# Optimization experiments

Hardware: AMD Instinct MI355X
Metric: run time of the kernel (lower is better)

Reference implementation:

```python
import jax, jax.numpy as jnp
import numpy as np

B, N = 128, 64
HID, MLP, DS, DV = 128, 128, 32, 32
DH = MLP - DS - DV  # 64
FILL = -10.0


def _embed_mask(x, W, b, fill):
    # Linear+ReLU on non-NaN rows; fill NaN rows with `fill` (matches embed_with_masking).
    nan = jnp.isnan(x).any(-1)
    e = jax.nn.relu(jnp.where(jnp.isnan(x), 0.0, x) @ W + b)
    return jnp.where(nan[..., None], jnp.asarray(fill, x.dtype), e)


def setup_inputs() -> dict:
    key = jax.random.key(0)
    ks = jax.random.split(key, 12)
    s = 0.05
    return {
        "hidden_states": jax.random.normal(ks[0], (B, N, HID), jnp.float32),
        "obs1": jax.random.normal(ks[1], (B, N, 2), jnp.float32),
        "obs2": jax.random.normal(ks[2], (B, N, 2), jnp.float32),
        "w_sp": jax.random.normal(ks[3], (2, DS), jnp.float32) * s,
        "b_sp": jnp.zeros((DS,), jnp.float32),
        "w_vel": jax.random.normal(ks[4], (2, DV), jnp.float32) * s,
        "b_vel": jnp.zeros((DV,), jnp.float32),
        "w_hid": jax.random.normal(ks[5], (HID, DH), jnp.float32) * s,
        "b_hid": jnp.zeros((DH,), jnp.float32),
        "wq": jax.random.normal(ks[6], (MLP, MLP), jnp.float32) * s,
        "wk": jax.random.normal(ks[7], (MLP, MLP), jnp.float32) * s,
        "wv": jax.random.normal(ks[8], (MLP, MLP), jnp.float32) * s,
        "in_proj_w": jax.random.normal(ks[9], (MLP, 3 * MLP), jnp.float32) * s,
        "in_proj_b": jnp.zeros((3 * MLP,), jnp.float32),
        "mha_out_w": jax.random.normal(ks[10], (MLP, MLP), jnp.float32) * s,
        "mha_out_b": jnp.zeros((MLP,), jnp.float32),
        "out_w": jax.random.normal(ks[11], (MLP, MLP), jnp.float32) * s,
        "out_b": jnp.zeros((MLP,), jnp.float32),
    }


def reference(hidden_states, obs1, obs2, w_sp, b_sp, w_vel, b_vel, w_hid, b_hid,
              wq, wk, wv, in_proj_w, in_proj_b, mha_out_w, mha_out_b, out_w, out_b):
    b, n = obs2.shape[0], obs2.shape[1]
    # relative positions: rel[b,i,j] = obs2[b,j] - obs2[b,i]
    rel = obs2[:, None, :, :] - obs2[:, :, None, :]              # [B,N,N,2]
    sp = _embed_mask(rel, w_sp, b_sp, FILL)                      # [B,N,N,DS]
    hid = _embed_mask(hidden_states, w_hid, b_hid, 0.0)          # [B,N,DH]
    hid_unf = jnp.broadcast_to(hid[:, None, :, :], (b, n, n, DH))
    vel = obs2 - obs1
    relvel = vel[:, None, :, :] - vel[:, :, None, :]             # [B,N,N,2]
    dv = _embed_mask(relvel * 4, w_vel, b_vel, FILL)             # [B,N,N,DV]
    emb = jnp.concatenate([sp, hid_unf, dv], axis=-1)            # [B,N,N,MLP]

    # MHA (1 head) in-proj weights split (stored as [in,out])
    w_iq, w_ik, w_iv = in_proj_w[:, :MLP], in_proj_w[:, MLP:2 * MLP], in_proj_w[:, 2 * MLP:]
    b_iq, b_ik, b_iv = in_proj_b[:MLP], in_proj_b[MLP:2 * MLP], in_proj_b[2 * MLP:]

    # Only the diagonal query position is kept by the final eye-mask gather,
    # and softmax rows are independent, so compute q only at j == i.
    idx = jnp.arange(n)
    emb_diag = emb[:, idx, idx]                                  # [B,N,MLP]
    q = (emb_diag @ wq) @ w_iq + b_iq                            # [B,N,MLP]
    k = (emb @ wk) @ w_ik + b_ik                                 # [B,N,N,MLP]
    v = (emb @ wv) @ w_iv + b_iv                                 # [B,N,N,MLP]

    scores = jnp.einsum('bid,bijd->bij', q, k) / jnp.sqrt(jnp.asarray(MLP, q.dtype))
    attn = jax.nn.softmax(scores, axis=-1)                       # [B,N,N]
    ctx = jnp.einsum('bij,bijd->bid', attn, v)                   # [B,N,MLP]
    mha_out = ctx @ mha_out_w + mha_out_b
    out = mha_out @ out_w + out_b                                # [B,N,out_dim]
    return out.reshape(b * n, -1)
```

## Files before the change

### kernel.cpp

```cpp
#include <hip/hip_runtime.h>

typedef float v2f __attribute__((ext_vector_type(2)));
#define PKFMA(a,b,c) __builtin_elementwise_fma((a),(b),(c))
#define PKMAX(a,b)   __builtin_elementwise_max((a),(b))
static __device__ __forceinline__ v2f vsplat(float s) { return (v2f){s, s}; }
static __device__ __forceinline__ v2f vmk(float a, float b) { return (v2f){a, b}; }
static __device__ __forceinline__ v2f shfl_xor_v2(v2f x, int m) {
    double d = __builtin_bit_cast(double, x);
    d = __shfl_xor(d, m, 64);
    return __builtin_bit_cast(v2f, d);
}

#define WS_WQC   0
#define WS_WKC   16384
#define WS_WVC   32768
#define WS_MOW   49152
#define WS_GQ    65536
#define WS_G0Q   73728
#define WS_FALL  73856
#define WS_FB    90240
#define WS_HID   90368
#define WS_NEED_HID_BYTES ((size_t)(90368 + 128*64*64) * 4)

__global__ __launch_bounds__(256) void precompute1(
    const float* __restrict__ wq, const float* __restrict__ wk,
    const float* __restrict__ wv, const float* __restrict__ in_proj_w,
    const float* __restrict__ mha_out_w, const float* __restrict__ out_w,
    const float* __restrict__ hs, const float* __restrict__ w_hid,
    const float* __restrict__ b_hid, float* __restrict__ ws)
{
    __shared__ __align__(16) float sbuf[4224];
    const int tid = threadIdx.x;

    if (blockIdx.x < 256) {
        const int mat  = blockIdx.x >> 6;
        const int rp   = blockIdx.x & 63;
        const int rsel = tid >> 7;
        const int col  = tid & 127;
        const int r    = 2 * rp + rsel;
        const float* A; const float* Bm; int ldb; float* C;
        if (mat == 0)      { A = wq;        Bm = in_proj_w;       ldb = 384; C = ws + WS_WQC; }
        else if (mat == 1) { A = wk;        Bm = in_proj_w + 128; ldb = 384; C = ws + WS_WKC; }
        else if (mat == 2) { A = wv;        Bm = in_proj_w + 256; ldb = 384; C = ws + WS_WVC; }
        else               { A = mha_out_w; Bm = out_w;           ldb = 128; C = ws + WS_MOW; }
        sbuf[tid] = A[r * 128 + col];
        __syncthreads();
        float acc = 0.f;
        #pragma unroll 8
        for (int d = 0; d < 128; ++d) acc = fmaf(sbuf[rsel * 128 + d], Bm[d * ldb + col], acc);
        C[r * 128 + col] = acc;
    } else {
        const int b2 = blockIdx.x - 256;
        const int b = b2 >> 1, half = b2 & 1;
        const float4* src = (const float4*)(hs + b * 8192 + half * 4096);
        for (int k = tid; k < 1024; k += 256) {
            const int row = k >> 5, c = k & 31;
            *(float4*)&sbuf[row * 132 + 4 * c] = src[k];
        }
        __syncthreads();
        const int ty = tid >> 4, tx = tid & 15;
        float a0c[4] = {0,0,0,0}, a1c[4] = {0,0,0,0};
        for (int d0 = 0; d0 < 128; d0 += 4) {
            const float4 a0 = *(const float4*)&sbuf[(2*ty+0)*132 + d0];
            const float4 a1 = *(const float4*)&sbuf[(2*ty+1)*132 + d0];
            const float* a0p = (const float*)&a0;
            const float* a1p = (const float*)&a1;
            #pragma unroll
            for (int dd = 0; dd < 4; ++dd) {
                const float4 w4 = *(const float4*)&w_hid[(d0+dd)*64 + 4*tx];
                a0c[0] = fmaf(a0p[dd], w4.x, a0c[0]); a0c[1] = fmaf(a0p[dd], w4.y, a0c[1]);
                a0c[2] = fmaf(a0p[dd], w4.z, a0c[2]); a0c[3] = fmaf(a0p[dd], w4.w, a0c[3]);
                a1c[0] = fmaf(a1p[dd], w4.x, a1c[0]); a1c[1] = fmaf(a1p[dd], w4.y, a1c[1]);
                a1c[2] = fmaf(a1p[dd], w4.z, a1c[2]); a1c[3] = fmaf(a1p[dd], w4.w, a1c[3]);
            }
        }
        const float4 bh = *(const float4*)&b_hid[4*tx];
        float* dst = ws + WS_HID + b * 4096 + (32*half + 2*ty) * 64 + 4*tx;
        *(float4*)dst        = make_float4(fmaxf(a0c[0]+bh.x,0.f), fmaxf(a0c[1]+bh.y,0.f),
                                           fmaxf(a0c[2]+bh.z,0.f), fmaxf(a0c[3]+bh.w,0.f));
        *(float4*)(dst + 64) = make_float4(fmaxf(a1c[0]+bh.x,0.f), fmaxf(a1c[1]+bh.y,0.f),
                                           fmaxf(a1c[2]+bh.z,0.f), fmaxf(a1c[3]+bh.w,0.f));
    }
}

__global__ __launch_bounds__(128) void precompute2(
    const float* __restrict__ b_sp, const float* __restrict__ b_vel,
    const float* __restrict__ in_proj_b, const float* __restrict__ mha_out_b,
    const float* __restrict__ out_w, const float* __restrict__ out_b,
    float* __restrict__ ws)
{
    const float* Wqc = ws + WS_WQC;
    const float* Wkc = ws + WS_WKC;
    const float* Wvc = ws + WS_WVC;
    const float* Mow = ws + WS_MOW;
    const int bid = blockIdx.x, tid = threadIdx.x;
    __shared__ __align__(16) float sa[128];

    if (bid < 64) {
        const int k = bid;
        sa[tid] = Wqc[(32 + k) * 128 + tid];
        __syncthreads();
        const int j = tid;
        const int pj = (j < 64) ? 32 + j : ((j < 96) ? j - 64 : j);
        const float* brow = Wkc + pj * 128;
        float acc = 0.f;
        #pragma unroll 8
        for (int d = 0; d < 128; d += 4) {
            const float4 a4 = *(const float4*)&sa[d];
            const float4 b4 = *(const float4*)&brow[d];
            acc = fmaf(a4.x, b4.x, fmaf(a4.y, b4.y, fmaf(a4.z, b4.z, fmaf(a4.w, b4.w, acc))));
        }
        ws[WS_GQ + k * 128 + j] = acc;
    } else if (bid < 192) {
        const int k2 = bid - 64;
        const int srcRow = (k2 < 32) ? k2 : ((k2 < 64) ? 96 + (k2 - 32) : 32 + (k2 - 64));
        sa[tid] = Wvc[srcRow * 128 + tid];
        __syncthreads();
        float acc = 0.f;
        #pragma unroll 8
        for (int m = 0; m < 128; ++m) acc = fmaf(sa[m], Mow[m * 128 + tid], acc);
        ws[WS_FALL + k2 * 128 + tid] = acc;
    } else if (bid == 192) {
        float acc = out_b[tid];
        #pragma unroll 8
        for (int m = 0; m < 128; ++m) {
            acc = fmaf(in_proj_b[256 + m], Mow[m * 128 + tid], acc);
            acc = fmaf(mha_out_b[m], out_w[m * 128 + tid], acc);
        }
        ws[WS_FB + tid] = acc;
    } else {
        float qc = in_proj_b[tid];
        #pragma unroll 4
        for (int s = 0; s < 32; ++s) {
            qc = fmaf(fmaxf(b_sp[s], 0.f),  Wqc[s * 128 + tid], qc);
            qc = fmaf(fmaxf(b_vel[s], 0.f), Wqc[(96 + s) * 128 + tid], qc);
        }
        sa[tid] = qc;
        __syncthreads();
        const int j = tid;
        const int pj = (j < 64) ? 32 + j : ((j < 96) ? j - 64 : j);
        const float* brow = Wkc + pj * 128;
        float acc = 0.f;
        #pragma unroll 8
        for (int d = 0; d < 128; d += 4) {
            const float4 a4 = *(const float4*)&sa[d];
            const float4 b4 = *(const float4*)&brow[d];
            acc = fmaf(a4.x, b4.x, fmaf(a4.y, b4.y, fmaf(a4.z, b4.z, fmaf(a4.w, b4.w, acc))));
        }
        ws[WS_G0Q + j] = acc;
    }
}

#define L_GQ   0
#define L_G0Q  8192
#define L_FALL 8320
#define L_FB   24704
#define L_HID  24832
#define L_OBS  29056
#define L_WV   29312
#define L_TOT  35456

template <bool HIDWS>
__global__ __launch_bounds__(512) void attn_main(
    const float* __restrict__ hs, const float* __restrict__ obs1,
    const float* __restrict__ obs2,
    const float* __restrict__ w_sp, const float* __restrict__ b_sp,
    const float* __restrict__ w_vel, const float* __restrict__ b_vel,
    const float* __restrict__ w_hid, const float* __restrict__ b_hid,
    const float* __restrict__ ws, float* __restrict__ out)
{
    const int tid = threadIdx.x;
    const int l   = tid & 63;
    const int w   = tid >> 6;
    const int b   = blockIdx.x >> 1;
    const int rg0 = (blockIdx.x & 1) * 32 + 4 * w;

    __shared__ __align__(16) float smem[L_TOT];
    float* const s_gq  = smem + L_GQ;
    float* const s_g0q = smem + L_G0Q;
    float* const s_fall= smem + L_FALL;
    float* const s_fb  = smem + L_FB;
    float* const s_hid = smem + L_HID;
    float* const s_obs = smem + L_OBS;
    float* const tt = smem + L_WV + w * 768;
    float* const qq = smem + L_WV + w * 768 + 256;
    float* const aa = smem + L_WV + w * 768 + 512;

    {
        const float4* src = (const float4*)(ws + WS_GQ);
        float4* dst = (float4*)smem;
        #pragma unroll
        for (int k = tid; k < 6208; k += 512) dst[k] = src[k];
    }
    if (tid < 64) {
        const int g = b * 64 + tid;
        const float2 o2 = ((const float2*)obs2)[g];
        const float2 o1 = ((const float2*)obs1)[g];
        *(float4*)&s_obs[tid * 4] = make_float4(o2.x, o2.y, o2.x - o1.x, o2.y - o1.y);
    }
    if (HIDWS) {
        const float4* src = (const float4*)(ws + WS_HID + b * 4096);
        #pragma unroll
        for (int k = tid; k < 1024; k += 512) {
            const int row = k >> 4, c4 = (k & 15) * 4;
            const float4 v = src[k];
            *(v2f*)&s_hid[row * 66 + c4]     = vmk(v.x, v.y);
            *(v2f*)&s_hid[row * 66 + c4 + 2] = vmk(v.z, v.w);
        }
    } else {
        const int r = tid >> 3, qseg = (tid & 7) * 8;
        float acc[8];
        #pragma unroll
        for (int c = 0; c < 8; ++c) acc[c] = b_hid[qseg + c];
        for (int k = 0; k < 128; ++k) {
            const float a = hs[b * 8192 + r * 128 + k];
            #pragma unroll
            for (int c4 = 0; c4 < 2; ++c4) {
                const float4 w4 = *(const float4*)&w_hid[k * 64 + qseg + 4 * c4];
                acc[4*c4+0] = fmaf(a, w4.x, acc[4*c4+0]);
                acc[4*c4+1] = fmaf(a, w4.y, acc[4*c4+1]);
                acc[4*c4+2] = fmaf(a, w4.z, acc[4*c4+2]);
                acc[4*c4+3] = fmaf(a, w4.w, acc[4*c4+3]);
            }
        }
        #pragma unroll
        for (int c = 0; c < 8; c += 2)
            *(v2f*)&s_hid[r * 66 + qseg + c] =
                vmk(fmaxf(acc[c], 0.f), fmaxf(acc[c+1], 0.f));
    }
    __syncthreads();

    {
        const v2f bias = *(const v2f*)&s_g0q[2 * l];
        v2f acc0 = bias, acc1 = bias, acc2 = bias, acc3 = bias;
        for (int k0 = 0; k0 < 64; k0 += 2) {
            const v2f g0 = *(const v2f*)&s_gq[k0 * 128 + 2 * l];
            const v2f g1 = *(const v2f*)&s_gq[(k0 + 1) * 128 + 2 * l];
            const v2f h0 = *(const v2f*)&s_hid[(rg0 + 0) * 66 + k0];
            const v2f h1 = *(const v2f*)&s_hid[(rg0 + 1) * 66 + k0];
            const v2f h2 = *(const v2f*)&s_hid[(rg0 + 2) * 66 + k0];
            const v2f h3 = *(const v2f*)&s_hid[(rg0 + 3) * 66 + k0];
            acc0 = PKFMA(vsplat(h0.x), g0, PKFMA(vsplat(h0.y), g1, acc0));
            acc1 = PKFMA(vsplat(h1.x), g0, PKFMA(vsplat(h1.y), g1, acc1));
            acc2 = PKFMA(vsplat(h2.x), g0, PKFMA(vsplat(h2.y), g1, acc2));
            acc3 = PKFMA(vsplat(h3.x), g0, PKFMA(vsplat(h3.y), g1, acc3));
        }
        if (l < 32) {
            const int c = 2 * l;
            *(v2f*)&tt[0 * 64 + c] = acc0;  *(v2f*)&tt[1 * 64 + c] = acc1;
            *(v2f*)&tt[2 * 64 + c] = acc2;  *(v2f*)&tt[3 * 64 + c] = acc3;
        } else {
            const int c = 2 * l - 64;
            *(v2f*)&qq[0 * 64 + c] = acc0;  *(v2f*)&qq[1 * 64 + c] = acc1;
            *(v2f*)&qq[2 * 64 + c] = acc2;  *(v2f*)&qq[3 * 64 + c] = acc3;
        }
    }

    float sc[4];
    {
        v2f s0 = (v2f){0.f,0.f}, s1 = s0, s2 = s0, s3 = s0;
        const float* hl = &s_hid[l * 66];
        for (int c0 = 0; c0 < 64; c0 += 2) {
            const v2f h2 = *(const v2f*)&hl[c0];
            s0 = PKFMA(*(const v2f*)&tt[0 * 64 + c0], h2, s0);
            s1 = PKFMA(*(const v2f*)&tt[1 * 64 + c0], h2, s1);
            s2 = PKFMA(*(const v2f*)&tt[2 * 64 + c0], h2, s2);
            s3 = PKFMA(*(const v2f*)&tt[3 * 64 + c0], h2, s3);
        }
        sc[0] = s0.x + s0.y; sc[1] = s1.x + s1.y;
        sc[2] = s2.x + s2.y; sc[3] = s3.x + s3.y;
    }

    {
        const float4 oj = *(const float4*)&s_obs[4 * l];
        float rx[4], ry[4], dx[4], dy[4];
        #pragma unroll
        for (int r = 0; r < 4; ++r) {
            const float4 oi = *(const float4*)&s_obs[4 * (rg0 + r)];
            rx[r] = oj.x - oi.x;  ry[r] = oj.y - oi.y;
            dx[r] = (oj.z - oi.z) * 4.f;  dy[r] = (oj.w - oi.w) * 4.f;
        }
        v2f acc[4] = {{0,0},{0,0},{0,0},{0,0}};
        for (int s0 = 0; s0 < 32; s0 += 2) {
            const v2f w0p = *(const v2f*)&w_sp[s0];
            const v2f w1p = *(const v2f*)&w_sp[32 + s0];
            const v2f bsp = *(const v2f*)&b_sp[s0];
            const v2f u0p = *(const v2f*)&w_vel[s0];
            const v2f u1p = *(const v2f*)&w_vel[32 + s0];
            const v2f bvp = *(const v2f*)&b_vel[s0];
            #pragma unroll
            for (int r = 0; r < 4; ++r) {
                const v2f qs2 = *(const v2f*)&qq[r * 64 + s0];
                const v2f qd2 = *(const v2f*)&qq[r * 64 + 32 + s0];
                const v2f esp = PKMAX(PKFMA(vsplat(rx[r]), w0p,
                                     PKFMA(vsplat(ry[r]), w1p, bsp)), vsplat(0.f));
                acc[r] = PKFMA(qs2, esp, acc[r]);
                const v2f edv = PKMAX(PKFMA(vsplat(dx[r]), u0p,
                                     PKFMA(vsplat(dy[r]), u1p, bvp)), vsplat(0.f));
                acc[r] = PKFMA(qd2, edv, acc[r]);
            }
        }
        const float scale = 0.08838834764831845f;
        v2f p01 = vmk((sc[0] + acc[0].x + acc[0].y) * scale,
                      (sc[1] + acc[1].x + acc[1].y) * scale);
        v2f p23 = vmk((sc[2] + acc[2].x + acc[2].y) * scale,
                      (sc[3] + acc[3].x + acc[3].y) * scale);
        v2f m01 = p01, m23 = p23;
        #pragma unroll
        for (int off = 32; off > 0; off >>= 1) {
            m01 = PKMAX(m01, shfl_xor_v2(m01, off));
            m23 = PKMAX(m23, shfl_xor_v2(m23, off));
        }
        v2f e01 = vmk(__expf(p01.x - m01.x), __expf(p01.y - m01.y));
        v2f e23 = vmk(__expf(p23.x - m23.x), __expf(p23.y - m23.y));
        v2f u01 = e01, u23 = e23;
        #pragma unroll
        for (int off = 32; off > 0; off >>= 1) {
            u01 = u01 + shfl_xor_v2(u01, off);
            u23 = u23 + shfl_xor_v2(u23, off);
        }
        *(float4*)&aa[4 * l] = make_float4(e01.x / u01.x, e01.y / u01.y,
                                           e23.x / u23.x, e23.y / u23.y);
    }

    {
        const int r = l >> 4, s = l & 15;
        const v2f w0p = vmk(w_sp[s],        w_sp[s + 16]);
        const v2f w1p = vmk(w_sp[32 + s],   w_sp[48 + s]);
        const v2f bsp = vmk(b_sp[s],        b_sp[s + 16]);
        const v2f u0p = vmk(w_vel[s],       w_vel[s + 16]);
        const v2f u1p = vmk(w_vel[32 + s],  w_vel[48 + s]);
        const v2f bvp = vmk(b_vel[s],       b_vel[s + 16]);
        const float4 oi = *(const float4*)&s_obs[4 * (rg0 + r)];
        v2f asp = (v2f){0.f, 0.f}, adv = asp;
        for (int j = 0; j < 64; ++j) {
            const float a = aa[4 * j + r];
            const float4 o4 = *(const float4*)&s_obs[4 * j];
            const float rxx = o4.x - oi.x, ryy = o4.y - oi.y;
            const float dxx = (o4.z - oi.z) * 4.f, dyy = (o4.w - oi.w) * 4.f;
            const v2f esp = PKMAX(PKFMA(vsplat(rxx), w0p,
                                 PKFMA(vsplat(ryy), w1p, bsp)), vsplat(0.f));
            asp = PKFMA(vsplat(a), esp, asp);
            const v2f edv = PKMAX(PKFMA(vsplat(dxx), u0p,
                                 PKFMA(vsplat(dyy), u1p, bvp)), vsplat(0.f));
            adv = PKFMA(vsplat(a), edv, adv);
        }
        tt[r * 64 + s]      = asp.x;
        tt[r * 64 + s + 16] = asp.y;
        tt[r * 64 + 32 + s] = adv.x;
        tt[r * 64 + 48 + s] = adv.y;
    }

    {
        float ah0 = 0.f, ah1 = 0.f, ah2 = 0.f, ah3 = 0.f;
        for (int j = 0; j < 64; j += 2) {
            const float4 a0 = *(const float4*)&aa[4 * j];
            const float4 a1 = *(const float4*)&aa[4 * j + 4];
            const float h0 = s_hid[j * 66 + l];
            const float h1 = s_hid[(j + 1) * 66 + l];
            ah0 = fmaf(a0.x, h0, fmaf(a1.x, h1, ah0));
            ah1 = fmaf(a0.y, h0, fmaf(a1.y, h1, ah1));
            ah2 = fmaf(a0.z, h0, fmaf(a1.z, h1, ah2));
            ah3 = fmaf(a0.w, h0, fmaf(a1.w, h1, ah3));
        }
        qq[0 * 64 + l] = ah0;  qq[1 * 64 + l] = ah1;
        qq[2 * 64 + l] = ah2;  qq[3 * 64 + l] = ah3;
    }

    {
        const v2f fb2 = *(const v2f*)&s_fb[2 * l];
        v2f o0 = fb2, o1 = fb2, o2 = fb2, o3 = fb2;
        for (int k = 0; k < 64; k += 2) {
            const v2f f0 = *(const v2f*)&s_fall[k * 128 + 2 * l];
            const v2f f1 = *(const v2f*)&s_fall[(k + 1) * 128 + 2 * l];
            const v2f A0 = *(const v2f*)&tt[0 * 64 + k];
            const v2f A1 = *(const v2f*)&tt[1 * 64 + k];
            const v2f A2 = *(const v2f*)&tt[2 * 64 + k];
            const v2f A3 = *(const v2f*)&tt[3 * 64 + k];
            o0 = PKFMA(vsplat(A0.x), f0, PKFMA(vsplat(A0.y), f1, o0));
            o1 = PKFMA(vsplat(A1.x), f0, PKFMA(vsplat(A1.y), f1, o1));
            o2 = PKFMA(vsplat(A2.x), f0, PKFMA(vsplat(A2.y), f1, o2));
            o3 = PKFMA(vsplat(A3.x), f0, PKFMA(vsplat(A3.y), f1, o3));
        }
        for (int k = 0; k < 64; k += 2) {
            const v2f f0 = *(const v2f*)&s_fall[(64 + k) * 128 + 2 * l];
            const v2f f1 = *(const v2f*)&s_fall[(65 + k) * 128 + 2 * l];
            const v2f A0 = *(const v2f*)&qq[0 * 64 + k];
            const v2f A1 = *(const v2f*)&qq[1 * 64 + k];
            const v2f A2 = *(const v2f*)&qq[2 * 64 + k];
            const v2f A3 = *(const v2f*)&qq[3 * 64 + k];
            o0 = PKFMA(vsplat(A0.x), f0, PKFMA(vsplat(A0.y), f1, o0));
            o1 = PKFMA(vsplat(A1.x), f0, PKFMA(vsplat(A1.y), f1, o1));
            o2 = PKFMA(vsplat(A2.x), f0, PKFMA(vsplat(A2.y), f1, o2));
            o3 = PKFMA(vsplat(A3.x), f0, PKFMA(vsplat(A3.y), f1, o3));
        }
        const int gr = (b * 64 + rg0) * 128 + 2 * l;
        *(v2f*)&out[gr]           = o0;
        *(v2f*)&out[gr + 128]     = o1;
        *(v2f*)&out[gr + 256]     = o2;
        *(v2f*)&out[gr + 384]     = o3;
    }
}

extern "C" void kernel_launch(void* const* d_in, const int* in_sizes, int n_in,
                              void* d_out, int out_size, void* d_ws, size_t ws_size,
                              hipStream_t stream) {
    const float* hs        = (const float*)d_in[0];
    const float* obs1      = (const float*)d_in[1];
    const float* obs2      = (const float*)d_in[2];
    const float* w_sp      = (const float*)d_in[3];
    const float* b_sp      = (const float*)d_in[4];
    const float* w_vel     = (const float*)d_in[5];
    const float* b_vel     = (const float*)d_in[6];
    const float* w_hid     = (const float*)d_in[7];
    const float* b_hid     = (const float*)d_in[8];
    const float* wq        = (const float*)d_in[9];
    const float* wk        = (const float*)d_in[10];
    const float* wv        = (const float*)d_in[11];
    const float* in_proj_w = (const float*)d_in[12];
    const float* in_proj_b = (const float*)d_in[13];
    const float* mha_out_w = (const float*)d_in[14];
    const float* mha_out_b = (const float*)d_in[15];
    const float* out_w     = (const float*)d_in[16];
    const float* out_b     = (const float*)d_in[17];
    float* ws  = (float*)d_ws;
    float* out = (float*)d_out;

    const bool hidws = (ws_size >= WS_NEED_HID_BYTES);

    precompute1<<<hidws ? 512 : 256, 256, 0, stream>>>(
        wq, wk, wv, in_proj_w, mha_out_w, out_w, hs, w_hid, b_hid, ws);
    precompute2<<<194, 128, 0, stream>>>(
        b_sp, b_vel, in_proj_b, mha_out_b, out_w, out_b, ws);
    if (hidws) {
        attn_main<true><<<256, 512, 0, stream>>>(hs, obs1, obs2, w_sp, b_sp, w_vel, b_vel,
                                                 w_hid, b_hid, ws, out);
    } else {
        attn_main<false><<<256, 512, 0, stream>>>(hs, obs1, obs2, w_sp, b_sp, w_vel, b_vel,
                                                  w_hid, b_hid, ws, out);
    }
}
```

Baseline: 125.8 us.

## Double attn_main block to 1024 threads with two query rows per wave

The main attention kernel now launches 1024 threads (16 waves) per block. Each wave handles 2 query rows instead of 4, and the per-wave scratch buffers shrink to match. The aggregation loop is also repacked so that the spatial and velocity embeddings share one packed FMA per lane, with 32 lanes per row. The aim is more waves to hide latency and more parallelism per block, since the grid is only 256 blocks. In exchange, the per-block LDS staging of the shared tables is amortized over fewer rows per wave, and 1024-thread blocks may cap registers per thread.

After: 126.6 us. About the same (+0.6%).

```diff
diff --git a/kernel.cpp b/kernel.cpp
--- a/kernel.cpp
+++ b/kernel.cpp
@@ -161,7 +161,7 @@
 #define L_TOT  35456
 
 template <bool HIDWS>
-__global__ __launch_bounds__(512) void attn_main(
+__global__ __launch_bounds__(1024) void attn_main(
     const float* __restrict__ hs, const float* __restrict__ obs1,
     const float* __restrict__ obs2,
     const float* __restrict__ w_sp, const float* __restrict__ b_sp,
@@ -173,7 +173,7 @@
     const int l   = tid & 63;
     const int w   = tid >> 6;
     const int b   = blockIdx.x >> 1;
-    const int rg0 = (blockIdx.x & 1) * 32 + 4 * w;
+    const int rg0 = (blockIdx.x & 1) * 32 + 2 * w;
 
     __shared__ __align__(16) float smem[L_TOT];
     float* const s_gq  = smem + L_GQ;
@@ -182,15 +182,15 @@
     float* const s_fb  = smem + L_FB;
     float* const s_hid = smem + L_HID;
     float* const s_obs = smem + L_OBS;
-    float* const tt = smem + L_WV + w * 768;
-    float* const qq = smem + L_WV + w * 768 + 256;
-    float* const aa = smem + L_WV + w * 768 + 512;
+    float* const tt = smem + L_WV + w * 384;
+    float* const qq = smem + L_WV + w * 384 + 128;
+    float* const aa = smem + L_WV + w * 384 + 256;
 
     {
         const float4* src = (const float4*)(ws + WS_GQ);
         float4* dst = (float4*)smem;
         #pragma unroll
-        for (int k = tid; k < 6208; k += 512) dst[k] = src[k];
+        for (int k = tid; k < 6208; k += 1024) dst[k] = src[k];
     }
     if (tid < 64) {
         const int g = b * 64 + tid;
@@ -200,87 +200,73 @@
     }
     if (HIDWS) {
         const float4* src = (const float4*)(ws + WS_HID + b * 4096);
-        #pragma unroll
-        for (int k = tid; k < 1024; k += 512) {
+        {
+            const int k = tid;
             const int row = k >> 4, c4 = (k & 15) * 4;
             const float4 v = src[k];
             *(v2f*)&s_hid[row * 66 + c4]     = vmk(v.x, v.y);
             *(v2f*)&s_hid[row * 66 + c4 + 2] = vmk(v.z, v.w);
         }
     } else {
-        const int r = tid >> 3, qseg = (tid & 7) * 8;
-        float acc[8];
-        #pragma unroll
-        for (int c = 0; c < 8; ++c) acc[c] = b_hid[qseg + c];
+        const int r = tid >> 4, c0 = (tid & 15) * 4;
+        float acc[4];
+        #pragma unroll
+        for (int c = 0; c < 4; ++c) acc[c] = b_hid[c0 + c];
         for (int k = 0; k < 128; ++k) {
             const float a = hs[b * 8192 + r * 128 + k];
-            #pragma unroll
-            for (int c4 = 0; c4 < 2; ++c4) {
-                const float4 w4 = *(const float4*)&w_hid[k * 64 + qseg + 4 * c4];
-                acc[4*c4+0] = fmaf(a, w4.x, acc[4*c4+0]);
-                acc[4*c4+1] = fmaf(a, w4.y, acc[4*c4+1]);
-                acc[4*c4+2] = fmaf(a, w4.z, acc[4*c4+2]);
-                acc[4*c4+3] = fmaf(a, w4.w, acc[4*c4+3]);
-            }
-        }
-        #pragma unroll
-        for (int c = 0; c < 8; c += 2)
-            *(v2f*)&s_hid[r * 66 + qseg + c] =
-                vmk(fmaxf(acc[c], 0.f), fmaxf(acc[c+1], 0.f));
+            const float4 w4 = *(const float4*)&w_hid[k * 64 + c0];
+            acc[0] = fmaf(a, w4.x, acc[0]);
+            acc[1] = fmaf(a, w4.y, acc[1]);
+            acc[2] = fmaf(a, w4.z, acc[2]);
+            acc[3] = fmaf(a, w4.w, acc[3]);
+        }
+        *(v2f*)&s_hid[r * 66 + c0]     = vmk(fmaxf(acc[0], 0.f), fmaxf(acc[1], 0.f));
+        *(v2f*)&s_hid[r * 66 + c0 + 2] = vmk(fmaxf(acc[2], 0.f), fmaxf(acc[3], 0.f));
     }
     __syncthreads();
 
     {
         const v2f bias = *(const v2f*)&s_g0q[2 * l];
-        v2f acc0 = bias, acc1 = bias, acc2 = bias, acc3 = bias;
+        v2f acc0 = bias, acc1 = bias;
         for (int k0 = 0; k0 < 64; k0 += 2) {
             const v2f g0 = *(const v2f*)&s_gq[k0 * 128 + 2 * l];
             const v2f g1 = *(const v2f*)&s_gq[(k0 + 1) * 128 + 2 * l];
             const v2f h0 = *(const v2f*)&s_hid[(rg0 + 0) * 66 + k0];
             const v2f h1 = *(const v2f*)&s_hid[(rg0 + 1) * 66 + k0];
-            const v2f h2 = *(const v2f*)&s_hid[(rg0 + 2) * 66 + k0];
-            const v2f h3 = *(const v2f*)&s_hid[(rg0 + 3) * 66 + k0];
             acc0 = PKFMA(vsplat(h0.x), g0, PKFMA(vsplat(h0.y), g1, acc0));
             acc1 = PKFMA(vsplat(h1.x), g0, PKFMA(vsplat(h1.y), g1, acc1));
-            acc2 = PKFMA(vsplat(h2.x), g0, PKFMA(vsplat(h2.y), g1, acc2));
-            acc3 = PKFMA(vsplat(h3.x), g0, PKFMA(vsplat(h3.y), g1, acc3));
         }
         if (l < 32) {
             const int c = 2 * l;
-            *(v2f*)&tt[0 * 64 + c] = acc0;  *(v2f*)&tt[1 * 64 + c] = acc1;
-            *(v2f*)&tt[2 * 64 + c] = acc2;  *(v2f*)&tt[3 * 64 + c] = acc3;
+            *(v2f*)&tt[c] = acc0;  *(v2f*)&tt[64 + c] = acc1;
         } else {
             const int c = 2 * l - 64;
-            *(v2f*)&qq[0 * 64 + c] = acc0;  *(v2f*)&qq[1 * 64 + c] = acc1;
-            *(v2f*)&qq[2 * 64 + c] = acc2;  *(v2f*)&qq[3 * 64 + c] = acc3;
-        }
-    }
-
-    float sc[4];
-    {
-        v2f s0 = (v2f){0.f,0.f}, s1 = s0, s2 = s0, s3 = s0;
+            *(v2f*)&qq[c] = acc0;  *(v2f*)&qq[64 + c] = acc1;
+        }
+    }
+
+    float sc0, sc1;
+    {
+        v2f s0 = (v2f){0.f, 0.f}, s1 = s0;
         const float* hl = &s_hid[l * 66];
         for (int c0 = 0; c0 < 64; c0 += 2) {
             const v2f h2 = *(const v2f*)&hl[c0];
-            s0 = PKFMA(*(const v2f*)&tt[0 * 64 + c0], h2, s0);
-            s1 = PKFMA(*(const v2f*)&tt[1 * 64 + c0], h2, s1);
-            s2 = PKFMA(*(const v2f*)&tt[2 * 64 + c0], h2, s2);
-            s3 = PKFMA(*(const v2f*)&tt[3 * 64 + c0], h2, s3);
-        }
-        sc[0] = s0.x + s0.y; sc[1] = s1.x + s1.y;
-        sc[2] = s2.x + s2.y; sc[3] = s3.x + s3.y;
+            s0 = PKFMA(*(const v2f*)&tt[c0], h2, s0);
+            s1 = PKFMA(*(const v2f*)&tt[64 + c0], h2, s1);
+        }
+        sc0 = s0.x + s0.y;  sc1 = s1.x + s1.y;
     }
 
     {
         const float4 oj = *(const float4*)&s_obs[4 * l];
-        float rx[4], ry[4], dx[4], dy[4];
-        #pragma unroll
-        for (int r = 0; r < 4; ++r) {
+        float rx[2], ry[2], dx[2], dy[2];
+        #pragma unroll
+        for (int r = 0; r < 2; ++r) {
             const float4 oi = *(const float4*)&s_obs[4 * (rg0 + r)];
             rx[r] = oj.x - oi.x;  ry[r] = oj.y - oi.y;
             dx[r] = (oj.z - oi.z) * 4.f;  dy[r] = (oj.w - oi.w) * 4.f;
         }
-        v2f acc[4] = {{0,0},{0,0},{0,0},{0,0}};
+        v2f acc[2] = {{0,0},{0,0}};
         for (int s0 = 0; s0 < 32; s0 += 2) {
             const v2f w0p = *(const v2f*)&w_sp[s0];
             const v2f w1p = *(const v2f*)&w_sp[32 + s0];
@@ -289,7 +275,7 @@
             const v2f u1p = *(const v2f*)&w_vel[32 + s0];
             const v2f bvp = *(const v2f*)&b_vel[s0];
             #pragma unroll
-            for (int r = 0; r < 4; ++r) {
+            for (int r = 0; r < 2; ++r) {
                 const v2f qs2 = *(const v2f*)&qq[r * 64 + s0];
                 const v2f qd2 = *(const v2f*)&qq[r * 64 + 32 + s0];
                 const v2f esp = PKMAX(PKFMA(vsplat(rx[r]), w0p,
@@ -301,104 +287,73 @@
             }
         }
         const float scale = 0.08838834764831845f;
-        v2f p01 = vmk((sc[0] + acc[0].x + acc[0].y) * scale,
-                      (sc[1] + acc[1].x + acc[1].y) * scale);
-        v2f p23 = vmk((sc[2] + acc[2].x + acc[2].y) * scale,
-                      (sc[3] + acc[3].x + acc[3].y) * scale);
-        v2f m01 = p01, m23 = p23;
-        #pragma unroll
-        for (int off = 32; off > 0; off >>= 1) {
+        v2f p01 = vmk((sc0 + acc[0].x + acc[0].y) * scale,
+                      (sc1 + acc[1].x + acc[1].y) * scale);
+        v2f m01 = p01;
+        #pragma unroll
+        for (int off = 32; off > 0; off >>= 1)
             m01 = PKMAX(m01, shfl_xor_v2(m01, off));
-            m23 = PKMAX(m23, shfl_xor_v2(m23, off));
-        }
         v2f e01 = vmk(__expf(p01.x - m01.x), __expf(p01.y - m01.y));
-        v2f e23 = vmk(__expf(p23.x - m23.x), __expf(p23.y - m23.y));
-        v2f u01 = e01, u23 = e23;
-        #pragma unroll
-        for (int off = 32; off > 0; off >>= 1) {
+        v2f u01 = e01;
+        #pragma unroll
+        for (int off = 32; off > 0; off >>= 1)
             u01 = u01 + shfl_xor_v2(u01, off);
-            u23 = u23 + shfl_xor_v2(u23, off);
-        }
-        *(float4*)&aa[4 * l] = make_float4(e01.x / u01.x, e01.y / u01.y,
-                                           e23.x / u23.x, e23.y / u23.y);
-    }
-
-    {
-        const int r = l >> 4, s = l & 15;
-        const v2f w0p = vmk(w_sp[s],        w_sp[s + 16]);
-        const v2f w1p = vmk(w_sp[32 + s],   w_sp[48 + s]);
-        const v2f bsp = vmk(b_sp[s],        b_sp[s + 16]);
-        const v2f u0p = vmk(w_vel[s],       w_vel[s + 16]);
-        const v2f u1p = vmk(w_vel[32 + s],  w_vel[48 + s]);
-        const v2f bvp = vmk(b_vel[s],       b_vel[s + 16]);
+        *(v2f*)&aa[2 * l] = vmk(e01.x / u01.x, e01.y / u01.y);
+    }
+
+    {
+        const int r = l >> 5, s = l & 31;
+        const v2f wa = vmk(w_sp[s],      w_vel[s]);
+        const v2f wb = vmk(w_sp[32 + s], w_vel[32 + s]);
+        const v2f bb = vmk(b_sp[s],      b_vel[s]);
         const float4 oi = *(const float4*)&s_obs[4 * (rg0 + r)];
-        v2f asp = (v2f){0.f, 0.f}, adv = asp;
+        v2f a2 = (v2f){0.f, 0.f};
         for (int j = 0; j < 64; ++j) {
-            const float a = aa[4 * j + r];
+            const float a = aa[2 * j + r];
             const float4 o4 = *(const float4*)&s_obs[4 * j];
-            const float rxx = o4.x - oi.x, ryy = o4.y - oi.y;
-            const float dxx = (o4.z - oi.z) * 4.f, dyy = (o4.w - oi.w) * 4.f;
-            const v2f esp = PKMAX(PKFMA(vsplat(rxx), w0p,
-                                 PKFMA(vsplat(ryy), w1p, bsp)), vsplat(0.f));
-            asp = PKFMA(vsplat(a), esp, asp);
-            const v2f edv = PKMAX(PKFMA(vsplat(dxx), u0p,
-                                 PKFMA(vsplat(dyy), u1p, bvp)), vsplat(0.f));
-            adv = PKFMA(vsplat(a), edv, adv);
-        }
-        tt[r * 64 + s]      = asp.x;
-        tt[r * 64 + s + 16] = asp.y;
-        tt[r * 64 + 32 + s] = adv.x;
-        tt[r * 64 + 48 + s] = adv.y;
-    }
-
-    {
-        float ah0 = 0.f, ah1 = 0.f, ah2 = 0.f, ah3 = 0.f;
+            const v2f xx = vmk(o4.x - oi.x, (o4.z - oi.z) * 4.f);
+            const v2f yy = vmk(o4.y - oi.y, (o4.w - oi.w) * 4.f);
+            const v2f e2 = PKMAX(PKFMA(xx, wa, PKFMA(yy, wb, bb)), vsplat(0.f));
+            a2 = PKFMA(vsplat(a), e2, a2);
+        }
+        tt[r * 64 + s]      = a2.x;
+        tt[r * 64 + 32 + s] = a2.y;
+    }
+
+    {
+        v2f ah = (v2f){0.f, 0.f};
         for (int j = 0; j < 64; j += 2) {
-            const float4 a0 = *(const float4*)&aa[4 * j];
-            const float4 a1 = *(const float4*)&aa[4 * j + 4];
+            const v2f a0 = *(const v2f*)&aa[2 * j];
+            const v2f a1 = *(const v2f*)&aa[2 * j + 2];
             const float h0 = s_hid[j * 66 + l];
             const float h1 = s_hid[(j + 1) * 66 + l];
-            ah0 = fmaf(a0.x, h0, fmaf(a1.x, h1, ah0));
-            ah1 = fmaf(a0.y, h0, fmaf(a1.y, h1, ah1));
-            ah2 = fmaf(a0.z, h0, fmaf(a1.z, h1, ah2));
-            ah3 = fmaf(a0.w, h0, fmaf(a1.w, h1, ah3));
-        }
-        qq[0 * 64 + l] = ah0;  qq[1 * 64 + l] = ah1;
-        qq[2 * 64 + l] = ah2;  qq[3 * 64 + l] = ah3;
+            ah = PKFMA(a0, vsplat(h0), PKFMA(a1, vsplat(h1), ah));
+        }
+        qq[l] = ah.x;  qq[64 + l] = ah.y;
     }
 
     {
         const v2f fb2 = *(const v2f*)&s_fb[2 * l];
-        v2f o0 = fb2, o1 = fb2, o2 = fb2, o3 = fb2;
+        v2f o0 = fb2, o1 = fb2;
         for (int k = 0; k < 64; k += 2) {
             const v2f f0 = *(const v2f*)&s_fall[k * 128 + 2 * l];
             const v2f f1 = *(const v2f*)&s_fall[(k + 1) * 128 + 2 * l];
-            const v2f A0 = *(const v2f*)&tt[0 * 64 + k];
-            const v2f A1 = *(const v2f*)&tt[1 * 64 + k];
-            const v2f A2 = *(const v2f*)&tt[2 * 64 + k];
-            const v2f A3 = *(const v2f*)&tt[3 * 64 + k];
+            const v2f A0 = *(const v2f*)&tt[k];
+            const v2f A1 = *(const v2f*)&tt[64 + k];
             o0 = PKFMA(vsplat(A0.x), f0, PKFMA(vsplat(A0.y), f1, o0));
             o1 = PKFMA(vsplat(A1.x), f0, PKFMA(vsplat(A1.y), f1, o1));
-            o2 = PKFMA(vsplat(A2.x), f0, PKFMA(vsplat(A2.y), f1, o2));
-            o3 = PKFMA(vsplat(A3.x), f0, PKFMA(vsplat(A3.y), f1, o3));
         }
         for (int k = 0; k < 64; k += 2) {
             const v2f f0 = *(const v2f*)&s_fall[(64 + k) * 128 + 2 * l];
             const v2f f1 = *(const v2f*)&s_fall[(65 + k) * 128 + 2 * l];
-            const v2f A0 = *(const v2f*)&qq[0 * 64 + k];
-            const v2f A1 = *(const v2f*)&qq[1 * 64 + k];
-            const v2f A2 = *(const v2f*)&qq[2 * 64 + k];
-            const v2f A3 = *(const v2f*)&qq[3 * 64 + k];
+            const v2f A0 = *(const v2f*)&qq[k];
+            const v2f A1 = *(const v2f*)&qq[64 + k];
             o0 = PKFMA(vsplat(A0.x), f0, PKFMA(vsplat(A0.y), f1, o0));
             o1 = PKFMA(vsplat(A1.x), f0, PKFMA(vsplat(A1.y), f1, o1));
-            o2 = PKFMA(vsplat(A2.x), f0, PKFMA(vsplat(A2.y), f1, o2));
-            o3 = PKFMA(vsplat(A3.x), f0, PKFMA(vsplat(A3.y), f1, o3));
         }
         const int gr = (b * 64 + rg0) * 128 + 2 * l;
-        *(v2f*)&out[gr]           = o0;
-        *(v2f*)&out[gr + 128]     = o1;
-        *(v2f*)&out[gr + 256]     = o2;
-        *(v2f*)&out[gr + 384]     = o3;
+        *(v2f*)&out[gr]       = o0;
+        *(v2f*)&out[gr + 128] = o1;
     }
 }
 
@@ -433,10 +388,10 @@
     precompute2<<<194, 128, 0, stream>>>(
         b_sp, b_vel, in_proj_b, mha_out_b, out_w, out_b, ws);
     if (hidws) {
-        attn_main<true><<<256, 512, 0, stream>>>(hs, obs1, obs2, w_sp, b_sp, w_vel, b_vel,
-                                                 w_hid, b_hid, ws, out);
+        attn_main<true><<<256, 1024, 0, stream>>>(hs, obs1, obs2, w_sp, b_sp, w_vel, b_vel,
+                                                  w_hid, b_hid, ws, out);
     } else {
-        attn_main<false><<<256, 512, 0, stream>>>(hs, obs1, obs2, w_sp, b_sp, w_vel, b_vel,
-                                                  w_hid, b_hid, ws, out);
-    }
-}
+        attn_main<false><<<256, 1024, 0, stream>>>(hs, obs1, obs2, w_sp, b_sp, w_vel, b_vel,
+                                                   w_hid, b_hid, ws, out);
+    }
+}
```
